# Kernel optimization log

Hardware: AMD Instinct MI355X
Metric: run time of the kernel (lower is better)

## Reference

```python
import jax, jax.numpy as jnp
import numpy as np

LN_EPS = 1e-5

def setup_inputs() -> dict:
    key = jax.random.key(0)
    k1, k2, k3, k4 = jax.random.split(key, 4)
    B, N, F, O = 8, 2048, 256, 256
    x = jax.random.normal(k1, (B, N, F), dtype=jnp.float32)
    adj = jax.random.uniform(k2, (B, N, N), dtype=jnp.float32)
    # LayerNorm affine params
    gamma = jnp.ones((F,), jnp.float32)
    beta = jnp.zeros((F,), jnp.float32)
    # Linear weights stored as [in, out] (torch stores [out, in]; math identical)
    W_self = jax.random.normal(k3, (F, O), dtype=jnp.float32) * (1.0 / np.sqrt(F))
    W_neigh = jax.random.normal(k4, (F, O), dtype=jnp.float32) * (1.0 / np.sqrt(F))
    return {"x": x, "adj": adj, "gamma": gamma, "beta": beta,
            "W_self": W_self, "W_neigh": W_neigh}

def reference(x, adj, gamma, beta, W_self, W_neigh):
    # LayerNorm over last dim
    mu = jnp.mean(x, axis=-1, keepdims=True)
    var = jnp.mean(jnp.square(x - mu), axis=-1, keepdims=True)
    xn = (x - mu) * jax.lax.rsqrt(var + LN_EPS) * gamma + beta

    # Normalized Laplacian: I - D_out^{-1/2} A D_in^{-1/2}
    # out_degree = column sums (dim=1), in_degree = row sums (dim=2)
    d_out = jnp.sum(adj, axis=1)   # [B, N]
    d_in = jnp.sum(adj, axis=2)    # [B, N]
    s_out = jnp.where(d_out != 0, jax.lax.rsqrt(d_out), 0.0)
    s_in = jnp.where(d_in != 0, jax.lax.rsqrt(d_in), 0.0)
    # diag(s_out) @ A @ diag(s_in) == row/col elementwise rescale (no N^3 work)
    A_norm = s_out[:, :, None] * adj * s_in[:, None, :]
    eye = jnp.eye(adj.shape[1], dtype=adj.dtype)
    L = eye[None, :, :] - A_norm    # [B, N, N]

    neighbor = jnp.einsum('bij,bjf->bif', L, xn)   # [B, N, F]
    pre = xn @ W_self + neighbor @ W_neigh          # [B, N, O]
    return jax.nn.softplus(pre)
```

## Files before the change

kernel.cpp:

```cpp
#include <hip/hip_runtime.h>
#include <stdint.h>

#define B_ 8
#define N_ 2048
#define F_ 256

typedef unsigned short u16;
typedef __attribute__((ext_vector_type(8))) short bf16x8;
typedef __attribute__((ext_vector_type(4))) float f32x4;

__device__ __forceinline__ u16 f2bf(float f) {
    uint32_t u = __builtin_bit_cast(uint32_t, f);
    u += 0x7FFFu + ((u >> 16) & 1u);
    return (u16)(u >> 16);
}

__device__ __forceinline__ void gload_lds16(const void* g, void* lds_uniform_base) {
    __builtin_amdgcn_global_load_lds(
        (const __attribute__((address_space(1))) uint32_t*)g,
        (__attribute__((address_space(3))) uint32_t*)lds_uniform_base, 16, 0, 0);
}

__global__ __launch_bounds__(256) void k_deg(const float* __restrict__ adj,
                                             float* __restrict__ deg_row,
                                             float* __restrict__ deg_col) {
    const int b = blockIdx.y, panel = blockIdx.x;
    const int t = threadIdx.x, w = t >> 6, l = t & 63;
    const float* base = adj + ((size_t)b * N_ + (size_t)panel * 16) * N_ + t * 8;
    float c[8];
#pragma unroll
    for (int e = 0; e < 8; ++e) c[e] = 0.f;
    __shared__ float rs[16][4];
#pragma unroll 4
    for (int r = 0; r < 16; ++r) {
        const float4 v0 = *(const float4*)(base + (size_t)r * N_);
        const float4 v1 = *(const float4*)(base + (size_t)r * N_ + 4);
        c[0] += v0.x; c[1] += v0.y; c[2] += v0.z; c[3] += v0.w;
        c[4] += v1.x; c[5] += v1.y; c[6] += v1.z; c[7] += v1.w;
        float s = (v0.x + v0.y) + (v0.z + v0.w) + (v1.x + v1.y) + (v1.z + v1.w);
#pragma unroll
        for (int off = 32; off; off >>= 1) s += __shfl_xor(s, off);
        if (l == 0) rs[r][w] = s;
    }
    float* dc = deg_col + (size_t)b * N_ + t * 8;
#pragma unroll
    for (int e = 0; e < 8; ++e) atomicAdd(dc + e, c[e]);
    __syncthreads();
    if (t < 16)
        deg_row[(size_t)b * N_ + panel * 16 + t] = rs[t][0] + rs[t][1] + rs[t][2] + rs[t][3];
}

__global__ __launch_bounds__(256) void k_ln(const float* __restrict__ x,
                                            const float* __restrict__ gamma,
                                            const float* __restrict__ beta,
                                            const float* __restrict__ deg_row,
                                            u16* __restrict__ xn,
                                            u16* __restrict__ yT) {
    const int b = blockIdx.y, panel = blockIdx.x;
    const int t = threadIdx.x, w = t >> 6, l = t & 63;
    __shared__ u16 yt[256 * 34];
    float g[4], be[4];
#pragma unroll
    for (int m = 0; m < 4; ++m) { g[m] = gamma[l + 64 * m]; be[m] = beta[l + 64 * m]; }
    for (int rr = 0; rr < 8; ++rr) {
        const int jj = w * 8 + rr;
        const int j = panel * 32 + jj;
        const float* xp = x + ((size_t)b * N_ + j) * F_;
        float v[4], s = 0.f, ss = 0.f;
#pragma unroll
        for (int m = 0; m < 4; ++m) { v[m] = xp[l + 64 * m]; s += v[m]; ss += v[m] * v[m]; }
#pragma unroll
        for (int off = 32; off; off >>= 1) { s += __shfl_xor(s, off); ss += __shfl_xor(ss, off); }
        const float mu = s * (1.f / 256.f);
        const float var = ss * (1.f / 256.f) - mu * mu;
        const float rstd = rsqrtf(var + 1e-5f);
        const float d = deg_row[(size_t)b * N_ + j];
        const float sin_ = (d != 0.f) ? rsqrtf(d) : 0.f;
        u16* xnp = xn + ((size_t)b * N_ + j) * F_;
#pragma unroll
        for (int m = 0; m < 4; ++m) {
            const float xv = (v[m] - mu) * rstd * g[m] + be[m];
            xnp[l + 64 * m] = f2bf(xv);
            yt[(l + 64 * m) * 34 + jj] = f2bf(sin_ * xv);
        }
    }
    __syncthreads();
#pragma unroll
    for (int m2 = 0; m2 < 2; ++m2) {
        const int f = (t >> 1) + 128 * m2;
        const int jj0 = (t & 1) * 16;
        uint32_t vals[8];
#pragma unroll
        for (int e = 0; e < 8; ++e) vals[e] = *(const uint32_t*)&yt[f * 34 + jj0 + 2 * e];
        uint4* dst = (uint4*)(yT + ((size_t)b * F_ + f) * N_ + panel * 32 + jj0);
        dst[0] = make_uint4(vals[0], vals[1], vals[2], vals[3]);
        dst[1] = make_uint4(vals[4], vals[5], vals[6], vals[7]);
    }
}

__global__ __launch_bounds__(256) void k_wprep(const float* __restrict__ Ws,
                                               const float* __restrict__ Wn,
                                               u16* __restrict__ WcT,
                                               u16* __restrict__ WnT) {
    const int k = blockIdx.x, o = threadIdx.x;
    const float a = Ws[k * 256 + o], q = Wn[k * 256 + o];
    WcT[o * 256 + k] = f2bf(a + q);
    WnT[o * 256 + k] = f2bf(-q);
}

__global__ __launch_bounds__(512) void k_gemm1(const float* __restrict__ adj,
                                               const u16* __restrict__ yT,
                                               const float* __restrict__ deg_col,
                                               u16* __restrict__ z) {
    const int i = blockIdx.x;
    const int g = i & 7, s = i >> 3;
    const int bm = g * 16 + (s & 15);
    const int nt = s >> 4;
    const int b = bm >> 4, m = bm & 15;
    const int i0 = m * 128, f0 = nt * 128;
    const int t = threadIdx.x, w = t >> 6, l = t & 63;
    const int wr = w >> 2, wc = w & 3;
    alignas(16) __shared__ u16 As[128 * 32];
    alignas(16) __shared__ u16 Bs[128 * 32];
    f32x4 acc[4][2];
#pragma unroll
    for (int mi = 0; mi < 4; ++mi)
#pragma unroll
        for (int ni = 0; ni < 2; ++ni) acc[mi][ni] = (f32x4)0.f;

    const float* abase = adj + ((size_t)b * N_ + i0) * N_;
    const u16* ybase = yT + ((size_t)b * F_ + f0) * (size_t)N_;
    const int o = w * 1024 + l * 16;
    const int fr = o >> 6, jb = (o & 63) >> 1;

    for (int kt = 0; kt < 64; ++kt) {
        const int k0 = kt * 32;
        gload_lds16(ybase + (size_t)fr * N_ + k0 + jb, (char*)Bs + (w << 10));
#pragma unroll
        for (int q = 0; q < 2; ++q) {
            const int idx = t + 512 * q;
            const int row = idx >> 3, jq = idx & 7;
            const float4 v = *(const float4*)(abase + (size_t)row * N_ + k0 + jq * 4);
            const uint32_t u0 = (uint32_t)f2bf(v.x) | ((uint32_t)f2bf(v.y) << 16);
            const uint32_t u1 = (uint32_t)f2bf(v.z) | ((uint32_t)f2bf(v.w) << 16);
            *(uint2*)&As[row * 32 + jq * 4] = make_uint2(u0, u1);
        }
        __syncthreads();
        bf16x8 af[4], bfr[2];
#pragma unroll
        for (int mi = 0; mi < 4; ++mi)
            af[mi] = *(const bf16x8*)&As[(wr * 64 + mi * 16 + (l & 15)) * 32 + (l >> 4) * 8];
#pragma unroll
        for (int ni = 0; ni < 2; ++ni)
            bfr[ni] = *(const bf16x8*)&Bs[(wc * 32 + ni * 16 + (l & 15)) * 32 + (l >> 4) * 8];
#pragma unroll
        for (int mi = 0; mi < 4; ++mi)
#pragma unroll
            for (int ni = 0; ni < 2; ++ni)
                acc[mi][ni] = __builtin_amdgcn_mfma_f32_16x16x32_bf16(af[mi], bfr[ni], acc[mi][ni], 0, 0, 0);
        __syncthreads();
    }
#pragma unroll
    for (int mi = 0; mi < 4; ++mi) {
#pragma unroll
        for (int r = 0; r < 4; ++r) {
            const int row = i0 + wr * 64 + mi * 16 + (l >> 4) * 4 + r;
            const float d = deg_col[(size_t)b * N_ + row];
            const float so = (d != 0.f) ? rsqrtf(d) : 0.f;
#pragma unroll
            for (int ni = 0; ni < 2; ++ni) {
                const int col = f0 + wc * 32 + ni * 16 + (l & 15);
                z[((size_t)b * N_ + row) * F_ + col] = f2bf(so * acc[mi][ni][r]);
            }
        }
    }
}

__global__ __launch_bounds__(512) void k_gemm2(const u16* __restrict__ xn,
                                               const u16* __restrict__ z,
                                               const u16* __restrict__ WcT,
                                               const u16* __restrict__ WnT,
                                               float* __restrict__ out) {
    const int i = blockIdx.x;
    const int g = i & 7, s = i >> 3;
    const int mt = g * 16 + (s & 15);
    const int nt = s >> 4;
    const int r0 = mt * 128, o0 = nt * 128;
    const int t = threadIdx.x, w = t >> 6, l = t & 63;
    const int wr = w >> 2, wc = w & 3;
    alignas(16) __shared__ u16 As[128 * 32];
    alignas(16) __shared__ u16 Bs[128 * 32];
    f32x4 acc[4][2];
#pragma unroll
    for (int mi = 0; mi < 4; ++mi)
#pragma unroll
        for (int ni = 0; ni < 2; ++ni) acc[mi][ni] = (f32x4)0.f;

    const int o = w * 1024 + l * 16;
    const int row = o >> 6, cb = (o & 63) >> 1;

    for (int kt = 0; kt < 16; ++kt) {
        const u16* asrc = (kt < 8) ? xn : z;
        const u16* bsrc = (kt < 8) ? WcT : WnT;
        const int kk0 = (kt & 7) * 32;
        gload_lds16(asrc + (size_t)(r0 + row) * F_ + kk0 + cb, (char*)As + (w << 10));
        gload_lds16(bsrc + (size_t)(o0 + row) * F_ + kk0 + cb, (char*)Bs + (w << 10));
        __syncthreads();
        bf16x8 af[4], bfr[2];
#pragma unroll
        for (int mi = 0; mi < 4; ++mi)
            af[mi] = *(const bf16x8*)&As[(wr * 64 + mi * 16 + (l & 15)) * 32 + (l >> 4) * 8];
#pragma unroll
        for (int ni = 0; ni < 2; ++ni)
            bfr[ni] = *(const bf16x8*)&Bs[(wc * 32 + ni * 16 + (l & 15)) * 32 + (l >> 4) * 8];
#pragma unroll
        for (int mi = 0; mi < 4; ++mi)
#pragma unroll
            for (int ni = 0; ni < 2; ++ni)
                acc[mi][ni] = __builtin_amdgcn_mfma_f32_16x16x32_bf16(af[mi], bfr[ni], acc[mi][ni], 0, 0, 0);
        __syncthreads();
    }
#pragma unroll
    for (int mi = 0; mi < 4; ++mi) {
#pragma unroll
        for (int r = 0; r < 4; ++r) {
            const int rr = r0 + wr * 64 + mi * 16 + (l >> 4) * 4 + r;
#pragma unroll
            for (int ni = 0; ni < 2; ++ni) {
                const int cc = o0 + wc * 32 + ni * 16 + (l & 15);
                const float p = acc[mi][ni][r];
                out[(size_t)rr * F_ + cc] = (p > 20.f) ? p : log1pf(expf(p));
            }
        }
    }
}

extern "C" void kernel_launch(void* const* d_in, const int* in_sizes, int n_in,
                              void* d_out, int out_size, void* d_ws, size_t ws_size,
                              hipStream_t stream) {
    (void)in_sizes; (void)n_in; (void)out_size; (void)ws_size;
    const float* x     = (const float*)d_in[0];
    const float* adj   = (const float*)d_in[1];
    const float* gamma = (const float*)d_in[2];
    const float* beta  = (const float*)d_in[3];
    const float* Ws    = (const float*)d_in[4];
    const float* Wn    = (const float*)d_in[5];
    float* out = (float*)d_out;

    char* ws = (char*)d_ws;
    float* deg_row = (float*)(ws + 0);
    float* deg_col = (float*)(ws + 65536);
    u16* xn  = (u16*)(ws + 131072);
    u16* yT  = (u16*)(ws + 131072 + 8388608);
    u16* z   = (u16*)(ws + 131072 + 2 * 8388608);
    u16* WcT = (u16*)(ws + 131072 + 3 * 8388608);
    u16* WnT = (u16*)(ws + 131072 + 3 * 8388608 + 131072);

    hipMemsetAsync(ws, 0, 131072, stream);
    k_deg  <<<dim3(128, 8), 256, 0, stream>>>(adj, deg_row, deg_col);
    k_wprep<<<256, 256, 0, stream>>>(Ws, Wn, WcT, WnT);
    k_ln   <<<dim3(64, 8), 256, 0, stream>>>(x, gamma, beta, deg_row, xn, yT);
    k_gemm1<<<256, 512, 0, stream>>>(adj, yT, deg_col, z);
    k_gemm2<<<256, 512, 0, stream>>>(xn, z, WcT, WnT, out);
}
```

Baseline: 379.1 us.

## Replace column-degree atomics with partial sums and remap GEMM block order

The degree kernel now handles 32-row panels and writes per-panel partial column sums to a scratch buffer aliased onto z. A new small kernel then reduces these partials into deg_col, which removes the global atomicAdds and the workspace memset. Both GEMM kernels also change how block index maps to tile, putting batches or M tiles across XCDs differently to change L2 locality. The cost is an extra kernel launch plus a 4 MB partial-sum write and read.

```diff
diff --git a/kernel.cpp b/kernel.cpp
--- a/kernel.cpp
+++ b/kernel.cpp
@@ -23,31 +23,42 @@
 
 __global__ __launch_bounds__(256) void k_deg(const float* __restrict__ adj,
                                              float* __restrict__ deg_row,
-                                             float* __restrict__ deg_col) {
+                                             float* __restrict__ pcol) {
     const int b = blockIdx.y, panel = blockIdx.x;
     const int t = threadIdx.x, w = t >> 6, l = t & 63;
-    const float* base = adj + ((size_t)b * N_ + (size_t)panel * 16) * N_ + t * 8;
-    float c[8];
-#pragma unroll
-    for (int e = 0; e < 8; ++e) c[e] = 0.f;
-    __shared__ float rs[16][4];
+    const float* base = adj + ((size_t)b * N_ + (size_t)panel * 32) * N_;
+    float c0[4], c1[4];
+#pragma unroll
+    for (int e = 0; e < 4; ++e) { c0[e] = 0.f; c1[e] = 0.f; }
+    __shared__ float rs[32][4];
 #pragma unroll 4
-    for (int r = 0; r < 16; ++r) {
-        const float4 v0 = *(const float4*)(base + (size_t)r * N_);
-        const float4 v1 = *(const float4*)(base + (size_t)r * N_ + 4);
-        c[0] += v0.x; c[1] += v0.y; c[2] += v0.z; c[3] += v0.w;
-        c[4] += v1.x; c[5] += v1.y; c[6] += v1.z; c[7] += v1.w;
+    for (int r = 0; r < 32; ++r) {
+        const float4 v0 = *(const float4*)(base + (size_t)r * N_ + t * 4);
+        const float4 v1 = *(const float4*)(base + (size_t)r * N_ + 1024 + t * 4);
+        c0[0] += v0.x; c0[1] += v0.y; c0[2] += v0.z; c0[3] += v0.w;
+        c1[0] += v1.x; c1[1] += v1.y; c1[2] += v1.z; c1[3] += v1.w;
         float s = (v0.x + v0.y) + (v0.z + v0.w) + (v1.x + v1.y) + (v1.z + v1.w);
 #pragma unroll
         for (int off = 32; off; off >>= 1) s += __shfl_xor(s, off);
         if (l == 0) rs[r][w] = s;
     }
-    float* dc = deg_col + (size_t)b * N_ + t * 8;
-#pragma unroll
-    for (int e = 0; e < 8; ++e) atomicAdd(dc + e, c[e]);
+    float4* pc = (float4*)(pcol + ((size_t)(b * 64 + panel)) * N_);
+    pc[t]       = make_float4(c0[0], c0[1], c0[2], c0[3]);
+    pc[t + 256] = make_float4(c1[0], c1[1], c1[2], c1[3]);
     __syncthreads();
-    if (t < 16)
-        deg_row[(size_t)b * N_ + panel * 16 + t] = rs[t][0] + rs[t][1] + rs[t][2] + rs[t][3];
+    if (t < 32)
+        deg_row[(size_t)b * N_ + panel * 32 + t] = rs[t][0] + rs[t][1] + rs[t][2] + rs[t][3];
+}
+
+__global__ __launch_bounds__(256) void k_dcol(const float* __restrict__ pcol,
+                                              float* __restrict__ deg_col) {
+    const int tid = blockIdx.x * 256 + threadIdx.x;
+    const int b = tid >> 11, j = tid & 2047;
+    const float* p = pcol + (size_t)b * 64 * N_ + j;
+    float s = 0.f;
+#pragma unroll
+    for (int g = 0; g < 64; ++g) s += p[(size_t)g * N_];
+    deg_col[tid] = s;
 }
 
 __global__ __launch_bounds__(256) void k_ln(const float* __restrict__ x,
@@ -113,10 +124,10 @@
                                                const float* __restrict__ deg_col,
                                                u16* __restrict__ z) {
     const int i = blockIdx.x;
-    const int g = i & 7, s = i >> 3;
-    const int bm = g * 16 + (s & 15);
-    const int nt = s >> 4;
-    const int b = bm >> 4, m = bm & 15;
+    const int b = i & 7;
+    const int kk = i >> 3;
+    const int nt = kk & 1;
+    const int m = kk >> 1;
     const int i0 = m * 128, f0 = nt * 128;
     const int t = threadIdx.x, w = t >> 6, l = t & 63;
     const int wr = w >> 2, wc = w & 3;
@@ -182,9 +193,10 @@
                                                const u16* __restrict__ WnT,
                                                float* __restrict__ out) {
     const int i = blockIdx.x;
-    const int g = i & 7, s = i >> 3;
-    const int mt = g * 16 + (s & 15);
-    const int nt = s >> 4;
+    const int xcd = i & 7;
+    const int kk = i >> 3;
+    const int nt = kk & 1;
+    const int mt = xcd + 8 * (kk >> 1);
     const int r0 = mt * 128, o0 = nt * 128;
     const int t = threadIdx.x, w = t >> 6, l = t & 63;
     const int wr = w >> 2, wc = w & 3;
@@ -255,9 +267,10 @@
     u16* z   = (u16*)(ws + 131072 + 2 * 8388608);
     u16* WcT = (u16*)(ws + 131072 + 3 * 8388608);
     u16* WnT = (u16*)(ws + 131072 + 3 * 8388608 + 131072);
-
-    hipMemsetAsync(ws, 0, 131072, stream);
-    k_deg  <<<dim3(128, 8), 256, 0, stream>>>(adj, deg_row, deg_col);
+    float* pcol = (float*)z;
+
+    k_deg  <<<dim3(64, 8), 256, 0, stream>>>(adj, deg_row, pcol);
+    k_dcol <<<64, 256, 0, stream>>>(pcol, deg_col);
     k_wprep<<<256, 256, 0, stream>>>(Ws, Wn, WcT, WnT);
     k_ln   <<<dim3(64, 8), 256, 0, stream>>>(x, gamma, beta, deg_row, xn, yT);
     k_gemm1<<<256, 512, 0, stream>>>(adj, yT, deg_col, z);
```

Result: faster. 323.5 us (-14.7%).
